# Kernel optimization log

Measured on AMD Instinct MI355X. Metric: run time of the kernel, lower is better.

## Reference

```python
import jax, jax.numpy as jnp
import numpy as np
from functools import partial

# Block hyperparams (match init_kwargs)
B, C, N, H = 16, 512, 1024, 8
HID = 4 * C
TAU, THRESH, SG_SCALE = 2.0, 1.0, 5.0
ATTN_SCALE = 0.25
BN_EPS = 1e-5

# LIF spiking neuron (single-step, stateless): membrane v = x / tau, hard threshold
# forward; sigmoid surrogate gradient (scale=5.0) in backward.
@partial(jax.custom_vjp, nondiff_argnums=(1,))
def spike(u, scale):
    return (u >= 0.0).astype(u.dtype)

def _spike_fwd(u, scale):
    return spike(u, scale), u

def _spike_bwd(scale, u, g):
    s = jax.nn.sigmoid(scale * u)
    return (g * scale * s * (1.0 - s),)

spike.defvjp(_spike_fwd, _spike_bwd)

def lif(x):
    return spike(x / TAU - THRESH, SG_SCALE)

def conv1x1(x, w, b=None):
    # x: [B,C,N], w: [O,C] -> [B,O,N]
    y = jnp.einsum('oc,bcn->bon', w, x)
    return y if b is None else y + b[None, :, None]

def bn(x, g, b):
    # BatchNorm1d, training-mode batch stats over (batch, length), biased var
    m = jnp.mean(x, axis=(0, 2), keepdims=True)
    v = jnp.var(x, axis=(0, 2), keepdims=True)
    return (x - m) * jax.lax.rsqrt(v + BN_EPS) * g[None, :, None] + b[None, :, None]


def setup_inputs() -> dict:
    key = jax.random.key(0)
    ks = jax.random.split(key, 8)
    w = lambda k, o, i: jax.random.normal(k, (o, i), dtype=jnp.float32) * 0.02
    inp = {
        'x': jax.random.normal(ks[0], (B, C, N), dtype=jnp.float32),
        'q_w': w(ks[1], C, C), 'q_g': jnp.ones((C,), jnp.float32), 'q_b': jnp.zeros((C,), jnp.float32),
        'k_w': w(ks[2], C, C), 'k_g': jnp.ones((C,), jnp.float32), 'k_b': jnp.zeros((C,), jnp.float32),
        'v_w': w(ks[3], C, C), 'v_g': jnp.ones((C,), jnp.float32), 'v_b': jnp.zeros((C,), jnp.float32),
        'proj_w': w(ks[4], C, C), 'proj_bias': jnp.zeros((C,), jnp.float32),
        'proj_g': jnp.ones((C,), jnp.float32), 'proj_b': jnp.zeros((C,), jnp.float32),
        'fc1_w': w(ks[5], HID, C), 'fc1_bias': jnp.zeros((HID,), jnp.float32),
        'fc1_g': jnp.ones((HID,), jnp.float32), 'fc1_b': jnp.zeros((HID,), jnp.float32),
        'fc2_w': w(ks[6], C, HID), 'fc2_bias': jnp.zeros((C,), jnp.float32),
        'fc2_g': jnp.ones((C,), jnp.float32), 'fc2_b': jnp.zeros((C,), jnp.float32),
    }
    return inp


def reference(x, q_w, q_g, q_b, k_w, k_g, k_b, v_w, v_g, v_b,
              proj_w, proj_bias, proj_g, proj_b,
              fc1_w, fc1_bias, fc1_g, fc1_b, fc2_w, fc2_bias, fc2_g, fc2_b):
    Bb, Cc, Nn = x.shape
    D = Cc // H

    def heads(t):  # [B,C,N] -> [B,H,N,D]
        return t.transpose(0, 2, 1).reshape(Bb, Nn, H, D).transpose(0, 2, 1, 3)

    # spiking attention (no softmax): (Q K^T) V * 0.25
    q = heads(lif(bn(conv1x1(x, q_w), q_g, q_b)))
    k = heads(lif(bn(conv1x1(x, k_w), k_g, k_b)))
    v = heads(lif(bn(conv1x1(x, v_w), v_g, v_b)))
    scores = jnp.einsum('bhnd,bhmd->bhnm', q, k)            # [B,H,N,N]
    attn = jnp.einsum('bhnm,bhmd->bhnd', scores, v) * ATTN_SCALE
    a = attn.transpose(0, 1, 3, 2).reshape(Bb, Cc, Nn)       # [B,C,N]
    a = lif(a)
    a = lif(bn(conv1x1(a, proj_w, proj_bias), proj_g, proj_b))
    x = x + a                                                # residual 1

    # conv1x1-BN-LIF MLP
    h = lif(bn(conv1x1(x, fc1_w, fc1_bias), fc1_g, fc1_b))
    h = lif(bn(conv1x1(h, fc2_w, fc2_bias), fc2_g, fc2_b))
    return x + h                                             # residual 2
```

## Files before the change

kernel.cpp:

```cpp
#include <hip/hip_runtime.h>
#include <stdint.h>

#pragma clang fp contract(off)

#define BATCH 16
#define CCH   512
#define NLEN  1024
#define NH    8
#define DH    64

__device__ float pw128(const float* __restrict__ x) {
    float r0=x[0],r1=x[1],r2=x[2],r3=x[3],r4=x[4],r5=x[5],r6=x[6],r7=x[7];
    for (int i = 8; i < 128; i += 8) {
        r0 += x[i+0]; r1 += x[i+1]; r2 += x[i+2]; r3 += x[i+3];
        r4 += x[i+4]; r5 += x[i+5]; r6 += x[i+6]; r7 += x[i+7];
    }
    return ((r0+r1)+(r2+r3))+((r4+r5)+(r6+r7));
}
__device__ float pw128_sqdev(const float* __restrict__ x, float m) {
    float r0,r1,r2,r3,r4,r5,r6,r7;
    {
        float d;
        d = x[0]-m; r0 = d*d;  d = x[1]-m; r1 = d*d;
        d = x[2]-m; r2 = d*d;  d = x[3]-m; r3 = d*d;
        d = x[4]-m; r4 = d*d;  d = x[5]-m; r5 = d*d;
        d = x[6]-m; r6 = d*d;  d = x[7]-m; r7 = d*d;
    }
    for (int i = 8; i < 128; i += 8) {
        float d;
        d = x[i+0]-m; r0 += d*d;  d = x[i+1]-m; r1 += d*d;
        d = x[i+2]-m; r2 += d*d;  d = x[i+3]-m; r3 += d*d;
        d = x[i+4]-m; r4 += d*d;  d = x[i+5]-m; r5 += d*d;
        d = x[i+6]-m; r6 += d*d;  d = x[i+7]-m; r7 += d*d;
    }
    return ((r0+r1)+(r2+r3))+((r4+r5)+(r6+r7));
}

__global__ __launch_bounds__(64) void bn_stats_np_k(const float* __restrict__ Y, int O,
                                                    float2* __restrict__ st)
{
    const int o = blockIdx.x;
    const int t = threadIdx.x;
    const int bi = t >> 2, q = t & 3;
    __shared__ float part[64];
    __shared__ float msh;
    const float* p = Y + ((size_t)bi * O + o) * NLEN + q * 256;
    {
        float s0 = pw128(p), s1 = pw128(p + 128);
        part[t] = s0 + s1;
    }
    __syncthreads();
    if (t == 0) {
        float s = 0.0f;
        for (int b = 0; b < 16; ++b) {
            const float* pp = &part[b * 4];
            float v = (pp[0] + pp[1]) + (pp[2] + pp[3]);
            s = (b == 0) ? v : (s + v);
        }
        msh = s / 16384.0f;
    }
    __syncthreads();
    const float m = msh;
    {
        float s0 = pw128_sqdev(p, m), s1 = pw128_sqdev(p + 128, m);
        part[t] = s0 + s1;
    }
    __syncthreads();
    if (t == 0) {
        float s = 0.0f;
        for (int b = 0; b < 16; ++b) {
            const float* pp = &part[b * 4];
            float v = (pp[0] + pp[1]) + (pp[2] + pp[3]);
            s = (b == 0) ? v : (s + v);
        }
        float var = s / 16384.0f;
        float ve  = var + 1e-5f;
        float sq  = (float)sqrt((double)ve);
        float r   = (float)(1.0 / (double)sq);
        st[o] = make_float2(m, r);
    }
}

__device__ inline bool spike_f32(float y, float2 s, float g, float b) {
    float t1 = y - s.x;
    float t2 = t1 * s.y;
    float t3 = t2 * g;
    float t4 = t3 + b;
    float u  = t4 / 2.0f - 1.0f;
    return u >= 0.0f;
}

template<int MODE>
__global__ __launch_bounds__(256) void gemm_k(
    const float* __restrict__ W, const float* __restrict__ Xf, const uint8_t* __restrict__ Xs8,
    const float* __restrict__ bias, float* __restrict__ Y,
    int O, int Cin, int N)
{
    __shared__ float Ws[2][16][132];
    __shared__ float Xs[2][16][132];
    const int b = blockIdx.z;
    const size_t xbase = (size_t)b * Cin * N;
    float* Yb = Y + (size_t)b * O * N;
    const int o0 = blockIdx.y * 128;
    const int n0 = blockIdx.x * 128;
    const int t  = threadIdx.x;
    const int tx = t & 15;
    const int ty = t >> 4;

    const int wr = t >> 1;
    const int wk = (t & 1) << 3;
    const int xk = t >> 4;
    const int xc = (t & 15) << 3;

    float acc[8][8];
#pragma unroll
    for (int i = 0; i < 8; ++i)
#pragma unroll
        for (int j = 0; j < 8; ++j) acc[i][j] = 0.0f;

    float4 wA[2];
    float  xr[8];

    auto loadG = [&](int k0) {
        const float* wp = W + (size_t)(o0 + wr) * Cin + k0 + wk;
        wA[0] = *reinterpret_cast<const float4*>(wp);
        wA[1] = *reinterpret_cast<const float4*>(wp + 4);
        size_t off = xbase + (size_t)(k0 + xk) * N + n0 + xc;
        float4 v0 = *reinterpret_cast<const float4*>(Xf + off);
        float4 v1 = *reinterpret_cast<const float4*>(Xf + off + 4);
        if (MODE == 0) {
            xr[0]=v0.x; xr[1]=v0.y; xr[2]=v0.z; xr[3]=v0.w;
            xr[4]=v1.x; xr[5]=v1.y; xr[6]=v1.z; xr[7]=v1.w;
        } else {
            uchar4 u0 = *reinterpret_cast<const uchar4*>(Xs8 + off);
            uchar4 u1 = *reinterpret_cast<const uchar4*>(Xs8 + off + 4);
            xr[0]=v0.x+(float)u0.x; xr[1]=v0.y+(float)u0.y;
            xr[2]=v0.z+(float)u0.z; xr[3]=v0.w+(float)u0.w;
            xr[4]=v1.x+(float)u1.x; xr[5]=v1.y+(float)u1.y;
            xr[6]=v1.z+(float)u1.z; xr[7]=v1.w+(float)u1.w;
        }
    };
    auto stage = [&](int buf) {
        Ws[buf][wk+0][wr]=wA[0].x; Ws[buf][wk+1][wr]=wA[0].y;
        Ws[buf][wk+2][wr]=wA[0].z; Ws[buf][wk+3][wr]=wA[0].w;
        Ws[buf][wk+4][wr]=wA[1].x; Ws[buf][wk+5][wr]=wA[1].y;
        Ws[buf][wk+6][wr]=wA[1].z; Ws[buf][wk+7][wr]=wA[1].w;
        *reinterpret_cast<float4*>(&Xs[buf][xk][xc])     = make_float4(xr[0],xr[1],xr[2],xr[3]);
        *reinterpret_cast<float4*>(&Xs[buf][xk][xc + 4]) = make_float4(xr[4],xr[5],xr[6],xr[7]);
    };

    loadG(0);
    stage(0);
    __syncthreads();
    int cur = 0;
    for (int k0 = 0;;) {
        const int kn = k0 + 16;
        const bool more = kn < Cin;
        if (more) loadG(kn);
#pragma unroll
        for (int kk = 0; kk < 16; ++kk) {
            float4 a0 = *reinterpret_cast<const float4*>(&Ws[cur][kk][ty * 4]);
            float4 a1 = *reinterpret_cast<const float4*>(&Ws[cur][kk][64 + ty * 4]);
            float4 b0 = *reinterpret_cast<const float4*>(&Xs[cur][kk][tx * 4]);
            float4 b1 = *reinterpret_cast<const float4*>(&Xs[cur][kk][64 + tx * 4]);
            float av[8] = {a0.x,a0.y,a0.z,a0.w,a1.x,a1.y,a1.z,a1.w};
            float bv[8] = {b0.x,b0.y,b0.z,b0.w,b1.x,b1.y,b1.z,b1.w};
#pragma unroll
            for (int i = 0; i < 8; ++i)
#pragma unroll
                for (int j = 0; j < 8; ++j)
                    acc[i][j] = fmaf(av[i], bv[j], acc[i][j]);
        }
        if (!more) break;
        stage(cur ^ 1);
        __syncthreads();
        cur ^= 1;
        k0 = kn;
    }
#pragma unroll
    for (int half = 0; half < 2; ++half)
#pragma unroll
        for (int i = 0; i < 4; ++i) {
            const int r = half * 4 + i;
            const int o = o0 + half * 64 + ty * 4 + i;
            const float bb = bias ? bias[o] : 0.0f;
            float* yp = Yb + (size_t)o * N + n0;
            float4 r0, r1;
            r0.x = acc[r][0] + bb; r0.y = acc[r][1] + bb;
            r0.z = acc[r][2] + bb; r0.w = acc[r][3] + bb;
            r1.x = acc[r][4] + bb; r1.y = acc[r][5] + bb;
            r1.z = acc[r][6] + bb; r1.w = acc[r][7] + bb;
            *reinterpret_cast<float4*>(yp + tx * 4)      = r0;
            *reinterpret_cast<float4*>(yp + 64 + tx * 4) = r1;
        }
}

__global__ __launch_bounds__(256) void wt_k(const float* __restrict__ W, float* __restrict__ Wt,
                                            int O, int Cin)
{
    __shared__ float tile[32][33];
    const int k0 = blockIdx.x * 32, o0 = blockIdx.y * 32;
    const int tx = threadIdx.x & 31, ty = threadIdx.x >> 5;
#pragma unroll
    for (int j = 0; j < 4; ++j)
        tile[ty + 8*j][tx] = W[(size_t)(o0 + ty + 8*j) * Cin + k0 + tx];
    __syncthreads();
#pragma unroll
    for (int j = 0; j < 4; ++j)
        Wt[(size_t)(k0 + ty + 8*j) * O + o0 + tx] = tile[tx][ty + 8*j];
}

__global__ __launch_bounds__(256) void col_bits_k(const uint8_t* __restrict__ S,
                                                  unsigned long long* __restrict__ bits, int Cin)
{
    const int n0 = blockIdx.x * 64, kw = blockIdx.y, b = blockIdx.z;
    __shared__ uint8_t tile[64][64];
    const int t = threadIdx.x;
    const int r = t >> 2, cg = (t & 3) * 16;
    const uint8_t* src = S + ((size_t)b * Cin + kw * 64 + r) * NLEN + n0 + cg;
    *reinterpret_cast<uint4*>(&tile[r][cg]) = *reinterpret_cast<const uint4*>(src);
    __syncthreads();
    if (t < 64) {
        unsigned long long m = 0;
#pragma unroll
        for (int rr = 0; rr < 64; ++rr)
            m |= ((unsigned long long)(tile[rr][t] != 0)) << rr;
        bits[((size_t)b * NLEN + n0 + t) * (Cin >> 6) + kw] = m;
    }
}

__global__ __launch_bounds__(256) void sparse_gemm_k(
    const float* __restrict__ Wt, const unsigned long long* __restrict__ bits,
    const float* __restrict__ bias, float* __restrict__ Y, int Cin)
{
    const int wid  = (blockIdx.x << 2) + (threadIdx.x >> 6);
    const int lane = threadIdx.x & 63;
    const int b = wid >> 10, n = wid & 1023;
    const int W64 = Cin >> 6;
    float acc[8];
#pragma unroll
    for (int i = 0; i < 8; ++i) acc[i] = 0.0f;
    const unsigned long long* bp = bits + ((size_t)b * NLEN + n) * W64;
    for (int w = 0; w < W64; ++w) {
        unsigned long long m = bp[w];
        while (m) {
            const int bit = __builtin_ctzll(m);
            m &= m - 1;
            const int k = (w << 6) + bit;
            const float* wr = Wt + ((size_t)k << 9) + lane * 8;
            float4 w0 = *reinterpret_cast<const float4*>(wr);
            float4 w1 = *reinterpret_cast<const float4*>(wr + 4);
            acc[0] += w0.x; acc[1] += w0.y; acc[2] += w0.z; acc[3] += w0.w;
            acc[4] += w1.x; acc[5] += w1.y; acc[6] += w1.z; acc[7] += w1.w;
        }
    }
    const float* bq = bias + lane * 8;
    float4 b0 = *reinterpret_cast<const float4*>(bq);
    float4 b1 = *reinterpret_cast<const float4*>(bq + 4);
    float bi[8] = {b0.x, b0.y, b0.z, b0.w, b1.x, b1.y, b1.z, b1.w};
    float* yp = Y + ((size_t)b * 512 + lane * 8) * NLEN + n;
#pragma unroll
    for (int i = 0; i < 8; ++i)
        yp[(size_t)i * NLEN] = acc[i] + bi[i];
}

__global__ __launch_bounds__(256) void spike_pack_qkv_k(
    const float* __restrict__ Y, const float2* __restrict__ st,
    const float* __restrict__ gq, const float* __restrict__ gk, const float* __restrict__ gv,
    const float* __restrict__ bq, const float* __restrict__ bk, const float* __restrict__ bv,
    uint8_t* __restrict__ oq, uint8_t* __restrict__ ok, uint8_t* __restrict__ ov)
{
    const int nt = blockIdx.x, hs = blockIdx.y, b = blockIdx.z;
    const int tensor = hs >> 3, h = hs & 7;
    const float* g  = (tensor == 0) ? gq : (tensor == 1) ? gk : gv;
    const float* be = (tensor == 0) ? bq : (tensor == 1) ? bk : bv;
    uint8_t* outp   = (tensor == 0) ? oq : (tensor == 1) ? ok : ov;
    __shared__ uint8_t tile[64][68];
    const int t = threadIdx.x;
    {
        const int i = t & 63, dq = t >> 6;
#pragma unroll
        for (int p = 0; p < 16; ++p) {
            int d  = dq * 16 + p;
            int cf = hs * 64 + d;
            int cl = h * 64 + d;
            float y = Y[((size_t)b * 1536 + cf) * NLEN + nt * 64 + i];
            tile[d][i] = spike_f32(y, st[cf], g[cl], be[cl]) ? 1 : 0;
        }
    }
    __syncthreads();
    {
        const int d = t & 63, iq = t >> 6;
#pragma unroll
        for (int p = 0; p < 16; ++p) {
            int i = iq * 16 + p;
            outp[((size_t)(b * NH + h) * NLEN + nt * 64 + i) * DH + d] = tile[d][i];
        }
    }
}

__global__ __launch_bounds__(256) void ktv_k(const uint8_t* __restrict__ Kb, const uint8_t* __restrict__ Vb,
                                             float* __restrict__ M)
{
    const int bh = blockIdx.x;
    const uint8_t* kp = Kb + (size_t)bh * NLEN * DH;
    const uint8_t* vp = Vb + (size_t)bh * NLEN * DH;
    __shared__ float ks[64][68];
    __shared__ float vs[64][68];
    const int t = threadIdx.x;
    const int d2 = t & 63, g4 = t >> 6;
    float acc[16];
#pragma unroll
    for (int j = 0; j < 16; ++j) acc[j] = 0.f;

    for (int nc = 0; nc < NLEN; nc += 64) {
#pragma unroll
        for (int p = 0; p < 16; ++p) {
            int idx = t + p * 256;
            int r = idx >> 6, d = idx & 63;
            ks[r][d] = (float)kp[(size_t)(nc + r) * DH + d];
            vs[r][d] = (float)vp[(size_t)(nc + r) * DH + d];
        }
        __syncthreads();
        for (int n = 0; n < 64; ++n) {
            float vv = vs[n][d2];
#pragma unroll
            for (int j = 0; j < 16; ++j)
                acc[j] += ks[n][g4 * 16 + j] * vv;
        }
        __syncthreads();
    }
#pragma unroll
    for (int j = 0; j < 16; ++j)
        M[(size_t)bh * 4096 + (size_t)(g4 * 16 + j) * 64 + d2] = acc[j];
}

__global__ __launch_bounds__(256) void attn_spike_k(const uint8_t* __restrict__ Qb, const float* __restrict__ M,
                                                    uint8_t* __restrict__ A)
{
    const int nt = blockIdx.x, h = blockIdx.y, b = blockIdx.z;
    const int bh = b * NH + h;
    __shared__ float Ms[64][68];
    __shared__ float qs[64][65];
    const int t = threadIdx.x;
#pragma unroll
    for (int p = 0; p < 16; ++p) {
        int idx = t + p * 256;
        int r = idx >> 6, c = idx & 63;
        Ms[r][c] = M[(size_t)bh * 4096 + idx];
        qs[c][r] = (float)Qb[((size_t)bh * NLEN + nt * 64 + r) * DH + c];
    }
    __syncthreads();
    const int n = t & 63, dg = t >> 6;
    float acc[16];
#pragma unroll
    for (int j = 0; j < 16; ++j) acc[j] = 0.f;
    for (int d1 = 0; d1 < 64; ++d1) {
        float qv = qs[d1][n];
#pragma unroll
        for (int j = 0; j < 16; ++j)
            acc[j] += qv * Ms[d1][dg * 16 + j];
    }
#pragma unroll
    for (int j = 0; j < 16; ++j) {
        int d = dg * 16 + j;
        A[((size_t)b * CCH + h * 64 + d) * NLEN + nt * 64 + n] = (acc[j] >= 8.0f) ? 1 : 0;
    }
}

__global__ __launch_bounds__(256) void spike_store_k(
    const float* __restrict__ Y, const float2* __restrict__ st,
    const float* __restrict__ g, const float* __restrict__ bet,
    uint8_t* __restrict__ H, int Oc, int o_off, int Otot)
{
    size_t i4 = (size_t)blockIdx.x * 256 + threadIdx.x;
    size_t total = (size_t)BATCH * Oc * (NLEN / 4);
    if (i4 >= total) return;
    int n4 = (int)(i4 & 255);
    int o  = (int)((i4 >> 8) % Oc);
    int b  = (int)(i4 / ((size_t)256 * Oc));
    float4 y = reinterpret_cast<const float4*>(Y)[i4];
    float2 s = st[o];
    float gg = g[o], bb = bet[o];
    uchar4 r;
    r.x = spike_f32(y.x, s, gg, bb) ? 1 : 0;
    r.y = spike_f32(y.y, s, gg, bb) ? 1 : 0;
    r.z = spike_f32(y.z, s, gg, bb) ? 1 : 0;
    r.w = spike_f32(y.w, s, gg, bb) ? 1 : 0;
    *reinterpret_cast<uchar4*>(H + ((size_t)(b * Otot + o_off + o)) * NLEN + n4 * 4) = r;
}

__global__ __launch_bounds__(256) void final_k(
    const float* __restrict__ Y, const float2* __restrict__ st,
    const float* __restrict__ g, const float* __restrict__ bet,
    const float* __restrict__ x, const uint8_t* __restrict__ ares,
    float* __restrict__ Out)
{
    size_t i4 = (size_t)blockIdx.x * 256 + threadIdx.x;
    size_t total = (size_t)BATCH * CCH * (NLEN / 4);
    if (i4 >= total) return;
    int o = (int)((i4 >> 8) % CCH);
    float4 y  = reinterpret_cast<const float4*>(Y)[i4];
    float4 xv = reinterpret_cast<const float4*>(x)[i4];
    uchar4 av = reinterpret_cast<const uchar4*>(ares)[i4];
    float2 s = st[o];
    float gg = g[o], bb = bet[o];
    float4 r;
    {
        float x1;
        x1 = xv.x + (float)av.x; r.x = x1 + (spike_f32(y.x, s, gg, bb) ? 1.0f : 0.0f);
        x1 = xv.y + (float)av.y; r.y = x1 + (spike_f32(y.y, s, gg, bb) ? 1.0f : 0.0f);
        x1 = xv.z + (float)av.z; r.z = x1 + (spike_f32(y.z, s, gg, bb) ? 1.0f : 0.0f);
        x1 = xv.w + (float)av.w; r.w = x1 + (spike_f32(y.w, s, gg, bb) ? 1.0f : 0.0f);
    }
    reinterpret_cast<float4*>(Out)[i4] = r;
}

extern "C" void kernel_launch(void* const* d_in, const int* in_sizes, int n_in,
                              void* d_out, int out_size, void* d_ws, size_t ws_size,
                              hipStream_t stream)
{
    const float* x         = (const float*)d_in[0];
    const float* q_w       = (const float*)d_in[1];
    const float* q_g       = (const float*)d_in[2];
    const float* q_b       = (const float*)d_in[3];
    const float* k_w       = (const float*)d_in[4];
    const float* k_g       = (const float*)d_in[5];
    const float* k_b       = (const float*)d_in[6];
    const float* v_w       = (const float*)d_in[7];
    const float* v_g       = (const float*)d_in[8];
    const float* v_b       = (const float*)d_in[9];
    const float* proj_w    = (const float*)d_in[10];
    const float* proj_bias = (const float*)d_in[11];
    const float* proj_g    = (const float*)d_in[12];
    const float* proj_b    = (const float*)d_in[13];
    const float* fc1_w     = (const float*)d_in[14];
    const float* fc1_bias  = (const float*)d_in[15];
    const float* fc1_g     = (const float*)d_in[16];
    const float* fc1_b     = (const float*)d_in[17];
    const float* fc2_w     = (const float*)d_in[18];
    const float* fc2_bias  = (const float*)d_in[19];
    const float* fc2_g     = (const float*)d_in[20];
    const float* fc2_b     = (const float*)d_in[21];
    float* out = (float*)d_out;

    char* ws = (char*)d_ws;
    const size_t MiB = 1ull << 20;
    if (ws_size < 124 * MiB) return;

    float*    Yq    = (float*)(ws);
    float*    Af    = (float*)(ws);
    uint8_t*  ab    = (uint8_t*)(ws);
    uint8_t*  ares  = (uint8_t*)(ws + 64 * MiB);
    uint8_t*  hb    = (uint8_t*)(ws + 72 * MiB);
    uint8_t*  qb    = (uint8_t*)(ws + 96 * MiB);
    uint8_t*  kb    = (uint8_t*)(ws + 104 * MiB);
    uint8_t*  vb    = (uint8_t*)(ws + 112 * MiB);
    float*    Wt    = (float*)(ws + 104 * MiB);
    unsigned long long* bits = (unsigned long long*)(ws + 108 * MiB);
    float*    Wcat  = (float*)(ws + 120 * MiB);
    float*    Mbuf  = (float*)(ws + 120 * MiB);
    float2*   stats = (float2*)(ws + 123 * MiB);

    dim3 thr256(256);

    hipMemcpyAsync(Wcat,          q_w, (size_t)512 * 512 * 4, hipMemcpyDeviceToDevice, stream);
    hipMemcpyAsync(Wcat + 262144, k_w, (size_t)512 * 512 * 4, hipMemcpyDeviceToDevice, stream);
    hipMemcpyAsync(Wcat + 524288, v_w, (size_t)512 * 512 * 4, hipMemcpyDeviceToDevice, stream);
    gemm_k<0><<<dim3(8, 12, 16), thr256, 0, stream>>>(Wcat, x, nullptr, nullptr, Yq, 1536, 512, 1024);
    bn_stats_np_k<<<dim3(1536), dim3(64), 0, stream>>>(Yq, 1536, stats);
    spike_pack_qkv_k<<<dim3(16, 24, 16), thr256, 0, stream>>>(Yq, stats, q_g, k_g, v_g,
                                                              q_b, k_b, v_b, qb, kb, vb);

    ktv_k<<<dim3(128), thr256, 0, stream>>>(kb, vb, Mbuf);
    attn_spike_k<<<dim3(16, 8, 16), thr256, 0, stream>>>(qb, Mbuf, ab);

    wt_k<<<dim3(16, 16), thr256, 0, stream>>>(proj_w, Wt, 512, 512);
    col_bits_k<<<dim3(16, 8, 16), thr256, 0, stream>>>(ab, bits, 512);
    sparse_gemm_k<<<dim3(4096), thr256, 0, stream>>>(Wt, bits, proj_bias, Af, 512);
    bn_stats_np_k<<<dim3(512), dim3(64), 0, stream>>>(Af, 512, stats);
    spike_store_k<<<dim3(8192), thr256, 0, stream>>>(Af, stats, proj_g, proj_b, ares, 512, 0, 512);

    for (int ch = 0; ch < 2; ++ch) {
        gemm_k<2><<<dim3(8, 8, 16), thr256, 0, stream>>>(fc1_w + (size_t)ch * 1024 * 512, x, ares,
                                                         fc1_bias + ch * 1024, Af, 1024, 512, 1024);
        bn_stats_np_k<<<dim3(1024), dim3(64), 0, stream>>>(Af, 1024, stats);
        spike_store_k<<<dim3(16384), thr256, 0, stream>>>(Af, stats, fc1_g + ch * 1024, fc1_b + ch * 1024,
                                                          hb, 1024, ch * 1024, 2048);
    }

    wt_k<<<dim3(64, 16), thr256, 0, stream>>>(fc2_w, Wt, 512, 2048);
    col_bits_k<<<dim3(16, 32, 16), thr256, 0, stream>>>(hb, bits, 2048);
    sparse_gemm_k<<<dim3(4096), thr256, 0, stream>>>(Wt, bits, fc2_bias, Af, 2048);
    bn_stats_np_k<<<dim3(512), dim3(64), 0, stream>>>(Af, 512, stats);
    final_k<<<dim3(8192), thr256, 0, stream>>>(Af, stats, fc2_g, fc2_b, x, ares, out);
}
```

Measured before the change: 1.450 ms.

## Read transposed weights directly from global in dense GEMM and split K^T V reduction

The dense GEMM no longer stages weights in shared memory. It pre-transposes Q/K/V and fc1 weights with wt_k and reads the weight rows as float4 directly from global/L2 inside the inner loop. This halves LDS traffic and barrier-staged data, in exchange for per-thread global loads in the compute loop that rely on cache hits. Separately, the K^T V kernel is split into 8 sequence chunks across 1024 blocks plus a reduce kernel, replacing 128 long-running blocks to raise parallelism.

```diff
diff --git a/kernel.cpp b/kernel.cpp
--- a/kernel.cpp
+++ b/kernel.cpp
@@ -92,11 +92,10 @@
 
 template<int MODE>
 __global__ __launch_bounds__(256) void gemm_k(
-    const float* __restrict__ W, const float* __restrict__ Xf, const uint8_t* __restrict__ Xs8,
+    const float* __restrict__ Wt, const float* __restrict__ Xf, const uint8_t* __restrict__ Xs8,
     const float* __restrict__ bias, float* __restrict__ Y,
-    int O, int Cin, int N)
-{
-    __shared__ float Ws[2][16][132];
+    int O, int Cin, int N, int ldW)
+{
     __shared__ float Xs[2][16][132];
     const int b = blockIdx.z;
     const size_t xbase = (size_t)b * Cin * N;
@@ -107,8 +106,6 @@
     const int tx = t & 15;
     const int ty = t >> 4;
 
-    const int wr = t >> 1;
-    const int wk = (t & 1) << 3;
     const int xk = t >> 4;
     const int xc = (t & 15) << 3;
 
@@ -118,13 +115,9 @@
 #pragma unroll
         for (int j = 0; j < 8; ++j) acc[i][j] = 0.0f;
 
-    float4 wA[2];
-    float  xr[8];
-
-    auto loadG = [&](int k0) {
-        const float* wp = W + (size_t)(o0 + wr) * Cin + k0 + wk;
-        wA[0] = *reinterpret_cast<const float4*>(wp);
-        wA[1] = *reinterpret_cast<const float4*>(wp + 4);
+    float xr[8];
+
+    auto loadGX = [&](int k0) {
         size_t off = xbase + (size_t)(k0 + xk) * N + n0 + xc;
         float4 v0 = *reinterpret_cast<const float4*>(Xf + off);
         float4 v1 = *reinterpret_cast<const float4*>(Xf + off + 4);
@@ -140,39 +133,46 @@
             xr[6]=v1.z+(float)u1.z; xr[7]=v1.w+(float)u1.w;
         }
     };
-    auto stage = [&](int buf) {
-        Ws[buf][wk+0][wr]=wA[0].x; Ws[buf][wk+1][wr]=wA[0].y;
-        Ws[buf][wk+2][wr]=wA[0].z; Ws[buf][wk+3][wr]=wA[0].w;
-        Ws[buf][wk+4][wr]=wA[1].x; Ws[buf][wk+5][wr]=wA[1].y;
-        Ws[buf][wk+6][wr]=wA[1].z; Ws[buf][wk+7][wr]=wA[1].w;
+    auto stageX = [&](int buf) {
         *reinterpret_cast<float4*>(&Xs[buf][xk][xc])     = make_float4(xr[0],xr[1],xr[2],xr[3]);
         *reinterpret_cast<float4*>(&Xs[buf][xk][xc + 4]) = make_float4(xr[4],xr[5],xr[6],xr[7]);
     };
 
-    loadG(0);
-    stage(0);
+    const float* wbase = Wt + o0 + ty * 4;
+
+    loadGX(0);
+    stageX(0);
     __syncthreads();
     int cur = 0;
     for (int k0 = 0;;) {
         const int kn = k0 + 16;
         const bool more = kn < Cin;
-        if (more) loadG(kn);
-#pragma unroll
-        for (int kk = 0; kk < 16; ++kk) {
-            float4 a0 = *reinterpret_cast<const float4*>(&Ws[cur][kk][ty * 4]);
-            float4 a1 = *reinterpret_cast<const float4*>(&Ws[cur][kk][64 + ty * 4]);
-            float4 b0 = *reinterpret_cast<const float4*>(&Xs[cur][kk][tx * 4]);
-            float4 b1 = *reinterpret_cast<const float4*>(&Xs[cur][kk][64 + tx * 4]);
-            float av[8] = {a0.x,a0.y,a0.z,a0.w,a1.x,a1.y,a1.z,a1.w};
-            float bv[8] = {b0.x,b0.y,b0.z,b0.w,b1.x,b1.y,b1.z,b1.w};
-#pragma unroll
-            for (int i = 0; i < 8; ++i)
-#pragma unroll
-                for (int j = 0; j < 8; ++j)
-                    acc[i][j] = fmaf(av[i], bv[j], acc[i][j]);
+        if (more) loadGX(kn);
+#pragma unroll
+        for (int kq = 0; kq < 4; ++kq) {
+            float4 a0[4], a1[4];
+            const float* wrow = wbase + (size_t)(k0 + kq * 4) * ldW;
+#pragma unroll
+            for (int u = 0; u < 4; ++u) {
+                a0[u] = *reinterpret_cast<const float4*>(wrow + (size_t)u * ldW);
+                a1[u] = *reinterpret_cast<const float4*>(wrow + (size_t)u * ldW + 64);
+            }
+#pragma unroll
+            for (int u = 0; u < 4; ++u) {
+                const int kk = kq * 4 + u;
+                float4 b0 = *reinterpret_cast<const float4*>(&Xs[cur][kk][tx * 4]);
+                float4 b1 = *reinterpret_cast<const float4*>(&Xs[cur][kk][64 + tx * 4]);
+                float av[8] = {a0[u].x,a0[u].y,a0[u].z,a0[u].w,a1[u].x,a1[u].y,a1[u].z,a1[u].w};
+                float bv[8] = {b0.x,b0.y,b0.z,b0.w,b1.x,b1.y,b1.z,b1.w};
+#pragma unroll
+                for (int i = 0; i < 8; ++i)
+#pragma unroll
+                    for (int j = 0; j < 8; ++j)
+                        acc[i][j] = fmaf(av[i], bv[j], acc[i][j]);
+            }
         }
         if (!more) break;
-        stage(cur ^ 1);
+        stageX(cur ^ 1);
         __syncthreads();
         cur ^= 1;
         k0 = kn;
@@ -196,7 +196,7 @@
 }
 
 __global__ __launch_bounds__(256) void wt_k(const float* __restrict__ W, float* __restrict__ Wt,
-                                            int O, int Cin)
+                                            int O, int Cin, int o_off, int Otot)
 {
     __shared__ float tile[32][33];
     const int k0 = blockIdx.x * 32, o0 = blockIdx.y * 32;
@@ -207,7 +207,7 @@
     __syncthreads();
 #pragma unroll
     for (int j = 0; j < 4; ++j)
-        Wt[(size_t)(k0 + ty + 8*j) * O + o0 + tx] = tile[tx][ty + 8*j];
+        Wt[(size_t)(k0 + ty + 8*j) * Otot + o_off + o0 + tx] = tile[tx][ty + 8*j];
 }
 
 __global__ __launch_bounds__(256) void col_bits_k(const uint8_t* __restrict__ S,
@@ -299,10 +299,11 @@
     }
 }
 
-__global__ __launch_bounds__(256) void ktv_k(const uint8_t* __restrict__ Kb, const uint8_t* __restrict__ Vb,
-                                             float* __restrict__ M)
-{
-    const int bh = blockIdx.x;
+__global__ __launch_bounds__(256) void ktv_part_k(const uint8_t* __restrict__ Kb,
+                                                  const uint8_t* __restrict__ Vb,
+                                                  float* __restrict__ Mp)
+{
+    const int bh = blockIdx.x, ch = blockIdx.y;
     const uint8_t* kp = Kb + (size_t)bh * NLEN * DH;
     const uint8_t* vp = Vb + (size_t)bh * NLEN * DH;
     __shared__ float ks[64][68];
@@ -313,7 +314,7 @@
 #pragma unroll
     for (int j = 0; j < 16; ++j) acc[j] = 0.f;
 
-    for (int nc = 0; nc < NLEN; nc += 64) {
+    for (int nc = ch * 128; nc < ch * 128 + 128; nc += 64) {
 #pragma unroll
         for (int p = 0; p < 16; ++p) {
             int idx = t + p * 256;
@@ -332,7 +333,25 @@
     }
 #pragma unroll
     for (int j = 0; j < 16; ++j)
-        M[(size_t)bh * 4096 + (size_t)(g4 * 16 + j) * 64 + d2] = acc[j];
+        Mp[((size_t)ch * 128 + bh) * 4096 + (size_t)(g4 * 16 + j) * 64 + d2] = acc[j];
+}
+
+__global__ __launch_bounds__(256) void ktv_reduce_k(const float* __restrict__ Mp,
+                                                    float* __restrict__ M)
+{
+    const int bh = blockIdx.x;
+    const int t = threadIdx.x;
+#pragma unroll
+    for (int j = 0; j < 16; j += 4) {
+        const int idx = t * 16 + j;
+        float4 s = *reinterpret_cast<const float4*>(&Mp[(size_t)bh * 4096 + idx]);
+#pragma unroll
+        for (int c = 1; c < 8; ++c) {
+            float4 v = *reinterpret_cast<const float4*>(&Mp[((size_t)c * 128 + bh) * 4096 + idx]);
+            s.x += v.x; s.y += v.y; s.z += v.z; s.w += v.w;
+        }
+        *reinterpret_cast<float4*>(&M[(size_t)bh * 4096 + idx]) = s;
+    }
 }
 
 __global__ __launch_bounds__(256) void attn_spike_k(const uint8_t* __restrict__ Qb, const float* __restrict__ M,
@@ -451,6 +470,7 @@
     float*    Yq    = (float*)(ws);
     float*    Af    = (float*)(ws);
     uint8_t*  ab    = (uint8_t*)(ws);
+    float*    Mpart = (float*)(ws + 16 * MiB);
     uint8_t*  ares  = (uint8_t*)(ws + 64 * MiB);
     uint8_t*  hb    = (uint8_t*)(ws + 72 * MiB);
     uint8_t*  qb    = (uint8_t*)(ws + 96 * MiB);
@@ -458,38 +478,42 @@
     uint8_t*  vb    = (uint8_t*)(ws + 112 * MiB);
     float*    Wt    = (float*)(ws + 104 * MiB);
     unsigned long long* bits = (unsigned long long*)(ws + 108 * MiB);
-    float*    Wcat  = (float*)(ws + 120 * MiB);
+    float*    Wtq   = (float*)(ws + 120 * MiB);
     float*    Mbuf  = (float*)(ws + 120 * MiB);
     float2*   stats = (float2*)(ws + 123 * MiB);
 
     dim3 thr256(256);
 
-    hipMemcpyAsync(Wcat,          q_w, (size_t)512 * 512 * 4, hipMemcpyDeviceToDevice, stream);
-    hipMemcpyAsync(Wcat + 262144, k_w, (size_t)512 * 512 * 4, hipMemcpyDeviceToDevice, stream);
-    hipMemcpyAsync(Wcat + 524288, v_w, (size_t)512 * 512 * 4, hipMemcpyDeviceToDevice, stream);
-    gemm_k<0><<<dim3(8, 12, 16), thr256, 0, stream>>>(Wcat, x, nullptr, nullptr, Yq, 1536, 512, 1024);
+    wt_k<<<dim3(16, 16), thr256, 0, stream>>>(q_w, Wtq, 512, 512,    0, 1536);
+    wt_k<<<dim3(16, 16), thr256, 0, stream>>>(k_w, Wtq, 512, 512,  512, 1536);
+    wt_k<<<dim3(16, 16), thr256, 0, stream>>>(v_w, Wtq, 512, 512, 1024, 1536);
+    gemm_k<0><<<dim3(8, 12, 16), thr256, 0, stream>>>(Wtq, x, nullptr, nullptr, Yq,
+                                                      1536, 512, 1024, 1536);
     bn_stats_np_k<<<dim3(1536), dim3(64), 0, stream>>>(Yq, 1536, stats);
     spike_pack_qkv_k<<<dim3(16, 24, 16), thr256, 0, stream>>>(Yq, stats, q_g, k_g, v_g,
                                                               q_b, k_b, v_b, qb, kb, vb);
 
-    ktv_k<<<dim3(128), thr256, 0, stream>>>(kb, vb, Mbuf);
+    ktv_part_k<<<dim3(128, 8), thr256, 0, stream>>>(kb, vb, Mpart);
+    ktv_reduce_k<<<dim3(128), thr256, 0, stream>>>(Mpart, Mbuf);
     attn_spike_k<<<dim3(16, 8, 16), thr256, 0, stream>>>(qb, Mbuf, ab);
 
-    wt_k<<<dim3(16, 16), thr256, 0, stream>>>(proj_w, Wt, 512, 512);
+    wt_k<<<dim3(16, 16), thr256, 0, stream>>>(proj_w, Wt, 512, 512, 0, 512);
     col_bits_k<<<dim3(16, 8, 16), thr256, 0, stream>>>(ab, bits, 512);
     sparse_gemm_k<<<dim3(4096), thr256, 0, stream>>>(Wt, bits, proj_bias, Af, 512);
     bn_stats_np_k<<<dim3(512), dim3(64), 0, stream>>>(Af, 512, stats);
     spike_store_k<<<dim3(8192), thr256, 0, stream>>>(Af, stats, proj_g, proj_b, ares, 512, 0, 512);
 
+    wt_k<<<dim3(16, 64), thr256, 0, stream>>>(fc1_w, Wt, 2048, 512, 0, 2048);
     for (int ch = 0; ch < 2; ++ch) {
-        gemm_k<2><<<dim3(8, 8, 16), thr256, 0, stream>>>(fc1_w + (size_t)ch * 1024 * 512, x, ares,
-                                                         fc1_bias + ch * 1024, Af, 1024, 512, 1024);
+        gemm_k<2><<<dim3(8, 8, 16), thr256, 0, stream>>>(Wt + ch * 1024, x, ares,
+                                                         fc1_bias + ch * 1024, Af,
+                                                         1024, 512, 1024, 2048);
         bn_stats_np_k<<<dim3(1024), dim3(64), 0, stream>>>(Af, 1024, stats);
         spike_store_k<<<dim3(16384), thr256, 0, stream>>>(Af, stats, fc1_g + ch * 1024, fc1_b + ch * 1024,
                                                           hb, 1024, ch * 1024, 2048);
     }
 
-    wt_k<<<dim3(64, 16), thr256, 0, stream>>>(fc2_w, Wt, 512, 2048);
+    wt_k<<<dim3(64, 16), thr256, 0, stream>>>(fc2_w, Wt, 512, 2048, 0, 512);
     col_bits_k<<<dim3(16, 32, 16), thr256, 0, stream>>>(hb, bits, 2048);
     sparse_gemm_k<<<dim3(4096), thr256, 0, stream>>>(Wt, bits, fc2_bias, Af, 2048);
     bn_stats_np_k<<<dim3(512), dim3(64), 0, stream>>>(Af, 512, stats);
```

Measured after the change: 1.631 ms. 12.4% more time.
